# Optimization experiments

Measured on AMD Instinct MI355X. Metric: run time of the kernel, lower is better.

Reference implementation:

```python
import jax, jax.numpy as jnp
import numpy as np

C64 = jnp.complex64
N_WIRES = 4


def _rx_b(theta):  # theta: [b] -> [b,2,2]
    c = jnp.cos(theta / 2).astype(C64)
    s = (-1j * jnp.sin(theta / 2)).astype(C64)
    return jnp.stack([jnp.stack([c, s], -1), jnp.stack([s, c], -1)], -2)


def _ry_b(theta):
    c = jnp.cos(theta / 2).astype(C64)
    s = jnp.sin(theta / 2).astype(C64)
    return jnp.stack([jnp.stack([c, -s], -1), jnp.stack([s, c], -1)], -2)


def _rz_b(theta):
    em = jnp.exp(-1j * theta.astype(C64) / 2)
    ep = jnp.exp(1j * theta.astype(C64) / 2)
    z = jnp.zeros_like(em)
    return jnp.stack([jnp.stack([em, z], -1), jnp.stack([z, ep], -1)], -2)


def _crx_mat(theta):  # scalar -> [4,4]
    c = jnp.cos(theta / 2).astype(C64)
    s = (-1j * jnp.sin(theta / 2)).astype(C64)
    m = jnp.eye(4, dtype=C64)
    m = m.at[2, 2].set(c).at[3, 3].set(c).at[2, 3].set(s).at[3, 2].set(s)
    return m


def _apply_1q(state, U, w):
    # state: [b,2,2,2,2]; U: [b,2,2] (batched) or [2,2]
    s = jnp.moveaxis(state, w + 1, 1)
    sh = s.shape
    s = s.reshape(sh[0], 2, -1)
    if U.ndim == 3:
        s = jnp.einsum('bij,bjr->bir', U, s)
    else:
        s = jnp.einsum('ij,bjr->bir', U, s)
    return jnp.moveaxis(s.reshape(sh), 1, w + 1)


def _apply_2q(state, U, wa, wb):
    # state: [b,2,2,2,2]; U: [4,4]; wa = first wire (high bit of U index)
    s = jnp.moveaxis(state, (wa + 1, wb + 1), (1, 2))
    sh = s.shape
    s = s.reshape(sh[0], 4, -1)
    s = jnp.einsum('ij,bjr->bir', U, s)
    return jnp.moveaxis(s.reshape(sh), (1, 2), (wa + 1, wb + 1))


_H = (1.0 / np.sqrt(2.0)) * jnp.array([[1, 1], [1, -1]], dtype=C64)
_SX = 0.5 * jnp.array([[1 + 1j, 1 - 1j], [1 - 1j, 1 + 1j]], dtype=C64)
_CNOT = jnp.array([[1, 0, 0, 0], [0, 1, 0, 0], [0, 0, 0, 1], [0, 0, 1, 0]], dtype=C64)
_U12 = jnp.array([[1, 0, 0, 0], [0, 1, 0, 0], [0, 0, 0, 1j], [0, 0, -1j, 0]], dtype=C64)


def setup_inputs() -> dict:
    key = jax.random.key(0)
    k0, k1, k2, k3, k4 = jax.random.split(key, 5)
    bsz = 131072
    return {
        'x': jax.random.normal(k0, (bsz, 1, 24, 24), dtype=jnp.float32),
        'theta_rx0': jax.random.normal(k1, (1,), dtype=jnp.float32),
        'theta_ry0': jax.random.normal(k2, (1,), dtype=jnp.float32),
        'theta_rz0': jax.random.normal(k3, (1,), dtype=jnp.float32),
        'theta_crx0': jax.random.normal(k4, (1,), dtype=jnp.float32),
    }


def reference(x, theta_rx0, theta_ry0, theta_rz0, theta_crx0):
    b = x.shape[0]
    # avg_pool2d(kernel=6, stride=6) on 24x24 -> 4x4, flatten to 16 angles
    xp = x.reshape(b, 4, 6, 4, 6).mean(axis=(2, 4)).reshape(b, 16)
    # |0000> state
    state = jnp.zeros((b, 2, 2, 2, 2), dtype=C64).at[:, 0, 0, 0, 0].set(1.0)
    # encoder: rx*4, ry*4, rz*4, rx*4 on wires k % 4 with batched angles
    for k in range(4):
        state = _apply_1q(state, _rx_b(xp[:, k]), k)
    for k in range(4):
        state = _apply_1q(state, _ry_b(xp[:, 4 + k]), k)
    for k in range(4):
        state = _apply_1q(state, _rz_b(xp[:, 8 + k]), k)
    for k in range(4):
        state = _apply_1q(state, _rx_b(xp[:, 12 + k]), k)
    # trainable gates (shared scalar params)
    state = _apply_1q(state, _rx_b(theta_rx0)[0], 0)
    state = _apply_1q(state, _ry_b(theta_ry0)[0], 1)
    state = _apply_1q(state, _rz_b(theta_rz0)[0], 3)
    state = _apply_2q(state, _crx_mat(theta_crx0[0]), 0, 2)
    state = _apply_1q(state, _H, 3)
    state = _apply_1q(state, _SX, 2)
    state = _apply_2q(state, _CNOT, 3, 0)
    state = _apply_2q(state, _U12, 1, 2)
    # MeasureAll(PauliZ): <Z_w> per wire
    probs = state.real ** 2 + state.imag ** 2  # [b,2,2,2,2]
    zvals = jnp.array([1.0, -1.0], dtype=probs.dtype)
    exps = []
    for w in range(N_WIRES):
        shape = [1] + [2 if i == w else 1 for i in range(N_WIRES)]
        exps.append((probs * zvals.reshape(shape)).sum(axis=(1, 2, 3, 4)))
    z = jnp.stack(exps, axis=-1)  # [b,4]
    logits = z.reshape(b, 2, 2).sum(-1)  # [b,2]
    return jax.nn.log_softmax(logits, axis=1)
```

## Files before the change

### kernel.cpp

```cpp
#include <hip/hip_runtime.h>


#define GL2LDS(gp, lp)                                             \
  __builtin_amdgcn_global_load_lds(                                \
      (const __attribute__((address_space(1))) void*)(gp),         \
      (__attribute__((address_space(3))) void*)(lp), 16, 0, 0)
#define BAR() __builtin_amdgcn_s_barrier()
#define WAITVM(N) asm volatile("s_waitcnt vmcnt(" #N ")" ::: "memory")
#define WAITLGKM() asm volatile("s_waitcnt lgkmcnt(0)" ::: "memory")

#define NCHUNK 16
#define CH_F4 1152
#define STG_F 4608
#define XPS 132

__device__ __forceinline__ void cmul(float ar, float ai, float br, float bi,
                                     float& cr, float& ci) {
  cr = ar * br - ai * bi;
  ci = ar * bi + ai * br;
}

struct C2 { float r0, i0, r1, i1; };

__device__ __forceinline__ void g_rx(C2& v, float h) {
  float s, c; __sincosf(h, &s, &c);
  C2 n;
  n.r0 = c * v.r0 + s * v.i1;
  n.i0 = c * v.i0 - s * v.r1;
  n.r1 = c * v.r1 + s * v.i0;
  n.i1 = c * v.i1 - s * v.r0;
  v = n;
}
__device__ __forceinline__ void g_ry(C2& v, float h) {
  float s, c; __sincosf(h, &s, &c);
  C2 n;
  n.r0 = c * v.r0 - s * v.r1;
  n.i0 = c * v.i0 - s * v.i1;
  n.r1 = s * v.r0 + c * v.r1;
  n.i1 = s * v.i0 + c * v.i1;
  v = n;
}
__device__ __forceinline__ void g_rz(C2& v, float h) {
  float s, c; __sincosf(h, &s, &c);
  C2 n;
  n.r0 = c * v.r0 + s * v.i0;
  n.i0 = c * v.i0 - s * v.r0;
  n.r1 = c * v.r1 - s * v.i1;
  n.i1 = c * v.i1 + s * v.r1;
  v = n;
}

__global__ __launch_bounds__(256, 3)
void qfc_kernel(const float* __restrict__ x,
                const float* __restrict__ thrx,
                const float* __restrict__ thry,
                const float* __restrict__ thrz,
                const float* __restrict__ thcrx,
                float* __restrict__ out) {
  __shared__ float stage[2 * STG_F];
  __shared__ float xp[16 * XPS];

  const int t = threadIdx.x;
  const int w = t >> 6;
  const long long img0 = (long long)blockIdx.x * 128;
  const float4* __restrict__ base4 =
      reinterpret_cast<const float4*>(x) + img0 * 144;

  auto issue = [&](int c, int buf) {
    const float4* gsrc = base4 + c * CH_F4;
    float* lbase = stage + buf * STG_F;
#pragma unroll
    for (int k = 0; k < 4; ++k) {
      const int L = k * 256 + t;
      const int img = L / 144;
      const int g = L ^ (img & 7);
      GL2LDS(gsrc + g, lbase + (k * 256 + w * 64) * 4);
    }
    if (t < 128) {
      const int L = 1024 + t;
      const int img = L / 144;
      const int g = L ^ (img & 7);
      GL2LDS(gsrc + g, lbase + (1024 + w * 64) * 4);
    }
  };

  auto pool = [&](int c, int buf) {
    const float* lb = stage + buf * STG_F;
    const int img = t >> 5;
    const int p = (t & 31) >> 1;
    const int half = t & 1;
    const int r0 = p >> 2, c0 = p & 3;
    float sum = 0.f;
#pragma unroll
    for (int r = 0; r < 3; ++r) {
      const int row = r0 * 6 + half * 3 + r;
#pragma unroll
      for (int off = 0; off < 6; off += 2) {
        const int f = row * 24 + c0 * 6 + off;
        const int slot = (img * 144 + (f >> 2)) ^ img;
        const float2 v = *reinterpret_cast<const float2*>(lb + slot * 4 + (f & 3));
        sum += v.x + v.y;
      }
    }
    const float tot = sum + __shfl_xor(sum, 1, 64);
    if (half == 0) xp[p * XPS + c * 8 + img] = tot * (1.0f / 36.0f);
  };

  issue(0, 0);
  issue(1, 1);
  for (int c = 0; c < NCHUNK; ++c) {
    if (c < NCHUNK - 1) {
      if (w < 2) WAITVM(5); else WAITVM(4);
    } else {
      WAITVM(0);
    }
    BAR();
    pool(c, c & 1);
    BAR();
    if (c + 2 < NCHUNK) issue(c + 2, c & 1);
  }
  WAITLGKM();
  BAR();

  if (t < 128) {
    float a[16];
#pragma unroll
    for (int p = 0; p < 16; ++p) a[p] = xp[p * XPS + t];

    const float arx = thrx[0] * 0.5f;
    const float ary = thry[0] * 0.5f;
    const float arz = thrz[0] * 0.5f;
    const float acr = thcrx[0] * 0.5f;

    C2 v[4];
#pragma unroll
    for (int wi = 0; wi < 4; ++wi) {
      v[wi].r0 = 1.f; v[wi].i0 = 0.f; v[wi].r1 = 0.f; v[wi].i1 = 0.f;
      g_rx(v[wi], a[wi] * 0.5f);
      g_ry(v[wi], a[4 + wi] * 0.5f);
      g_rz(v[wi], a[8 + wi] * 0.5f);
      g_rx(v[wi], a[12 + wi] * 0.5f);
    }
    g_rx(v[0], arx);
    g_ry(v[1], ary);
    g_rz(v[3], arz);

    float t01r[4], t01i[4], t23r[4], t23i[4];
    cmul(v[0].r0, v[0].i0, v[1].r0, v[1].i0, t01r[0], t01i[0]);
    cmul(v[0].r0, v[0].i0, v[1].r1, v[1].i1, t01r[1], t01i[1]);
    cmul(v[0].r1, v[0].i1, v[1].r0, v[1].i0, t01r[2], t01i[2]);
    cmul(v[0].r1, v[0].i1, v[1].r1, v[1].i1, t01r[3], t01i[3]);
    cmul(v[2].r0, v[2].i0, v[3].r0, v[3].i0, t23r[0], t23i[0]);
    cmul(v[2].r0, v[2].i0, v[3].r1, v[3].i1, t23r[1], t23i[1]);
    cmul(v[2].r1, v[2].i1, v[3].r0, v[3].i0, t23r[2], t23i[2]);
    cmul(v[2].r1, v[2].i1, v[3].r1, v[3].i1, t23r[3], t23i[3]);

    float re[16], im[16];
#pragma unroll
    for (int hi = 0; hi < 4; ++hi)
#pragma unroll
      for (int lo = 0; lo < 4; ++lo)
        cmul(t01r[hi], t01i[hi], t23r[lo], t23i[lo], re[hi * 4 + lo], im[hi * 4 + lo]);

    {
      float s, cc2; __sincosf(acr, &s, &cc2);
#pragma unroll
      for (int k = 0; k < 4; ++k) {
        const int pi4[4] = {8, 9, 12, 13};
        int i = pi4[k], j = i + 2;
        float nir = cc2 * re[i] + s * im[j];
        float nii = cc2 * im[i] - s * re[j];
        float njr = cc2 * re[j] + s * im[i];
        float nji = cc2 * im[j] - s * re[i];
        re[i] = nir; im[i] = nii; re[j] = njr; im[j] = nji;
      }
    }
#pragma unroll
    for (int i = 0; i < 16; i += 2) {
      const float inv = 0.70710678118654752f;
      float ar = re[i], ai = im[i], br = re[i + 1], bi = im[i + 1];
      re[i] = (ar + br) * inv;     im[i] = (ai + bi) * inv;
      re[i + 1] = (ar - br) * inv; im[i + 1] = (ai - bi) * inv;
    }
#pragma unroll
    for (int i = 0; i < 16; ++i) {
      if ((i & 2) == 0) {
        int j = i + 2;
        float ar = re[i], ai = im[i], br = re[j], bi = im[j];
        re[i] = 0.5f * (ar - ai + br + bi);
        im[i] = 0.5f * (ar + ai - br + bi);
        re[j] = 0.5f * (ar + ai + br - bi);
        im[j] = 0.5f * (ai - ar + br + bi);
      }
    }
#pragma unroll
    for (int i = 1; i < 8; i += 2) {
      float tr = re[i], ti = im[i];
      re[i] = re[i + 8]; im[i] = im[i + 8];
      re[i + 8] = tr;    im[i + 8] = ti;
    }
#pragma unroll
    for (int k = 0; k < 4; ++k) {
      const int ii4[4] = {4, 5, 12, 13};
      int i = ii4[k], j = i + 2;
      float tr = re[i], ti = im[i];
      re[i] = -im[j]; im[i] = re[j];
      re[j] = ti;     im[j] = -tr;
    }

    float z0 = 0.f, z1 = 0.f, z2 = 0.f, z3 = 0.f;
#pragma unroll
    for (int i = 0; i < 16; ++i) {
      float p = re[i] * re[i] + im[i] * im[i];
      z0 += (i & 8) ? -p : p;
      z1 += (i & 4) ? -p : p;
      z2 += (i & 2) ? -p : p;
      z3 += (i & 1) ? -p : p;
    }
    float l0 = z0 + z1, l1 = z2 + z3;
    float m = fmaxf(l0, l1);
    float e0 = __expf(l0 - m), e1 = __expf(l1 - m);
    float lse = __logf(e0 + e1);
    float2 o;
    o.x = l0 - m - lse;
    o.y = l1 - m - lse;
    reinterpret_cast<float2*>(out)[img0 + t] = o;
  }
}

extern "C" void kernel_launch(void* const* d_in, const int* in_sizes, int n_in,
                              void* d_out, int out_size, void* d_ws, size_t ws_size,
                              hipStream_t stream) {
  const float* x = (const float*)d_in[0];
  const float* thrx = (const float*)d_in[1];
  const float* thry = (const float*)d_in[2];
  const float* thrz = (const float*)d_in[3];
  const float* thcrx = (const float*)d_in[4];
  float* out = (float*)d_out;
  qfc_kernel<<<1024, 256, 0, stream>>>(x, thrx, thry, thrz, thcrx, out);
}
```

Measured before the change: 57.04 us.

## Stage input through registers into padded LDS instead of direct global-to-LDS loads

After: 149.3 us. 2.62x slower.

```diff
diff --git a/kernel.cpp b/kernel.cpp
--- a/kernel.cpp
+++ b/kernel.cpp
@@ -1,17 +1,12 @@
 #include <hip/hip_runtime.h>
 
 
-#define GL2LDS(gp, lp)                                             \
-  __builtin_amdgcn_global_load_lds(                                \
-      (const __attribute__((address_space(1))) void*)(gp),         \
-      (__attribute__((address_space(3))) void*)(lp), 16, 0, 0)
+#define LGKM() asm volatile("s_waitcnt lgkmcnt(0)" ::: "memory")
 #define BAR() __builtin_amdgcn_s_barrier()
-#define WAITVM(N) asm volatile("s_waitcnt vmcnt(" #N ")" ::: "memory")
-#define WAITLGKM() asm volatile("s_waitcnt lgkmcnt(0)" ::: "memory")
 
 #define NCHUNK 16
-#define CH_F4 1152
-#define STG_F 4608
+#define PADF 584
+#define STG_F 4672
 #define XPS 132
 
 __device__ __forceinline__ void cmul(float ar, float ai, float br, float bi,
@@ -61,66 +56,65 @@
   __shared__ float xp[16 * XPS];
 
   const int t = threadIdx.x;
-  const int w = t >> 6;
   const long long img0 = (long long)blockIdx.x * 128;
   const float4* __restrict__ base4 =
       reinterpret_cast<const float4*>(x) + img0 * 144;
 
-  auto issue = [&](int c, int buf) {
-    const float4* gsrc = base4 + c * CH_F4;
-    float* lbase = stage + buf * STG_F;
+  float4 rA[5], rB[5];
+
+  auto issue = [&](float4* r, int c) {
+    const float4* g = base4 + c * 1152 + t;
+#pragma unroll
+    for (int k = 0; k < 4; ++k) r[k] = g[k * 256];
+    if (t < 128) r[4] = g[1024];
+  };
+  auto put = [&](const float4* r, int buf) {
+    float* sp = stage + buf * STG_F;
 #pragma unroll
     for (int k = 0; k < 4; ++k) {
       const int L = k * 256 + t;
       const int img = L / 144;
-      const int g = L ^ (img & 7);
-      GL2LDS(gsrc + g, lbase + (k * 256 + w * 64) * 4);
+      const int off = L - img * 144;
+      *reinterpret_cast<float4*>(&sp[img * PADF + off * 4]) = r[k];
     }
     if (t < 128) {
       const int L = 1024 + t;
       const int img = L / 144;
-      const int g = L ^ (img & 7);
-      GL2LDS(gsrc + g, lbase + (1024 + w * 64) * 4);
+      const int off = L - img * 144;
+      *reinterpret_cast<float4*>(&sp[img * PADF + off * 4]) = r[4];
     }
   };
-
   auto pool = [&](int c, int buf) {
-    const float* lb = stage + buf * STG_F;
-    const int img = t >> 5;
-    const int p = (t & 31) >> 1;
-    const int half = t & 1;
-    const int r0 = p >> 2, c0 = p & 3;
-    float sum = 0.f;
-#pragma unroll
-    for (int r = 0; r < 3; ++r) {
-      const int row = r0 * 6 + half * 3 + r;
-#pragma unroll
-      for (int off = 0; off < 6; off += 2) {
-        const int f = row * 24 + c0 * 6 + off;
-        const int slot = (img * 144 + (f >> 2)) ^ img;
-        const float2 v = *reinterpret_cast<const float2*>(lb + slot * 4 + (f & 3));
-        sum += v.x + v.y;
+    if (t < 128) {
+      const int img = t >> 4;
+      const int p = t & 15;
+      const int r0 = p >> 2, c0 = p & 3;
+      const float* b = &stage[buf * STG_F + img * PADF + r0 * 144 + c0 * 6];
+      float sum = 0.f;
+#pragma unroll
+      for (int r = 0; r < 6; ++r) {
+        float2 a0 = *reinterpret_cast<const float2*>(b + r * 24);
+        float2 a1 = *reinterpret_cast<const float2*>(b + r * 24 + 2);
+        float2 a2 = *reinterpret_cast<const float2*>(b + r * 24 + 4);
+        sum += a0.x + a0.y + a1.x + a1.y + a2.x + a2.y;
       }
-    }
-    const float tot = sum + __shfl_xor(sum, 1, 64);
-    if (half == 0) xp[p * XPS + c * 8 + img] = tot * (1.0f / 36.0f);
+      xp[p * XPS + c * 8 + img] = sum * (1.0f / 36.0f);
+    }
   };
 
-  issue(0, 0);
-  issue(1, 1);
-  for (int c = 0; c < NCHUNK; ++c) {
-    if (c < NCHUNK - 1) {
-      if (w < 2) WAITVM(5); else WAITVM(4);
-    } else {
-      WAITVM(0);
-    }
-    BAR();
-    pool(c, c & 1);
-    BAR();
-    if (c + 2 < NCHUNK) issue(c + 2, c & 1);
+  issue(rA, 0);
+  issue(rB, 1);
+  for (int cc = 0; cc < NCHUNK; cc += 2) {
+    put(rA, 0);
+    if (cc + 2 < NCHUNK) issue(rA, cc + 2);
+    LGKM(); BAR();
+    pool(cc, 0);
+    put(rB, 1);
+    if (cc + 3 < NCHUNK) issue(rB, cc + 3);
+    LGKM(); BAR();
+    pool(cc + 1, 1);
   }
-  WAITLGKM();
-  BAR();
+  LGKM(); BAR();
 
   if (t < 128) {
     float a[16];
```
